# Kernel tuning notes

Hardware: AMD Instinct MI355X
Metric: run time of the kernel (lower is better)

The kernel has to match this reference:

```python
import jax, jax.numpy as jnp
import numpy as np

HID = 64
ENC_T = 20
DEC_T = 30


def lstm_cell(x, h, c, W_ih, W_hh, b_ih, b_hh):
    # PyTorch LSTMCell gate order: i, f, g, o
    gates = x @ W_ih.T + h @ W_hh.T + b_ih + b_hh  # [B, 4*HID]
    i, f, g, o = jnp.split(gates, 4, axis=-1)
    c_new = jax.nn.sigmoid(f) * c + jax.nn.sigmoid(i) * jnp.tanh(g)
    h_new = jax.nn.sigmoid(o) * jnp.tanh(c_new)
    return h_new, c_new


def setup_inputs() -> dict:
    key = jax.random.key(0)
    ks = jax.random.split(key, 11)
    B = 65536
    s_enc = 1.0 / np.sqrt(HID)
    u = lambda k, shape: jax.random.uniform(k, shape, jnp.float32, -s_enc, s_enc)
    return {
        "train_traj": jax.random.normal(ks[0], (B, ENC_T, 2), jnp.float32),
        "W_ih_enc": u(ks[1], (4 * HID, 2)),
        "W_hh_enc": u(ks[2], (4 * HID, HID)),
        "b_ih_enc": u(ks[3], (4 * HID,)),
        "b_hh_enc": u(ks[4], (4 * HID,)),
        "W_ih_dec": u(ks[5], (4 * HID, HID)),
        "W_hh_dec": u(ks[6], (4 * HID, HID)),
        "b_ih_dec": u(ks[7], (4 * HID,)),
        "b_hh_dec": u(ks[8], (4 * HID,)),
        "W_pos": u(ks[9], (2, HID)),
        "b_pos": u(ks[10], (2,)),
    }


def reference(train_traj, W_ih_enc, W_hh_enc, b_ih_enc, b_hh_enc,
              W_ih_dec, W_hh_dec, b_ih_dec, b_hh_dec, W_pos, b_pos):
    B = train_traj.shape[0]
    h0 = jnp.zeros((B, HID), train_traj.dtype)
    c0 = jnp.zeros((B, HID), train_traj.dtype)

    # Encoder: scan over the 20 time steps
    def enc_step(carry, x_t):
        h, c = carry
        h, c = lstm_cell(x_t, h, c, W_ih_enc, W_hh_enc, b_ih_enc, b_hh_enc)
        return (h, c), None

    xs = jnp.transpose(train_traj, (1, 0, 2))  # [T, B, 2]
    (h, c), _ = jax.lax.scan(enc_step, (h0, c0), xs)

    # Decoder: feed h back in as the input for 30 steps
    def dec_step(carry, _):
        h, c = carry
        h_new, c_new = lstm_cell(h, h, c, W_ih_dec, W_hh_dec, b_ih_dec, b_hh_dec)
        out = h_new @ W_pos.T + b_pos  # [B, 2]
        return (h_new, c_new), out

    (_, _), outs = jax.lax.scan(dec_step, (h, c), None, length=DEC_T)
    return jnp.transpose(outs, (1, 0, 2))  # [B, 30, 2]
```

## Files before the change

### kernel.cpp

```cpp
#include <hip/hip_runtime.h>

#define HID   64
#define ENC_T 20
#define DEC_T 30
#define ROWS  32
#define HS    72

typedef _Float16 f16;
typedef _Float16 f16x8 __attribute__((ext_vector_type(8)));
typedef _Float16 f16x4 __attribute__((ext_vector_type(4)));
typedef float  f32x4  __attribute__((ext_vector_type(4)));
typedef float  f32x2  __attribute__((ext_vector_type(2)));
typedef unsigned int   uint_t;

#if __has_builtin(__builtin_amdgcn_exp2f)
#define EXP2F(x) __builtin_amdgcn_exp2f(x)
#else
#define EXP2F(x) exp2f(x)
#endif
#if __has_builtin(__builtin_amdgcn_rcpf)
#define RCPF(x) __builtin_amdgcn_rcpf(x)
#else
#define RCPF(x) (1.0f / (x))
#endif

#define L2E 1.4426950408889634f

__device__ __forceinline__ f32x2 exp2_2(f32x2 x) {
    f32x2 r; r[0] = EXP2F(x[0]); r[1] = EXP2F(x[1]); return r;
}
__device__ __forceinline__ void batch_inv4_pk(f32x2 D0, f32x2 D1, f32x2 D2, f32x2 D3,
                                              f32x2& i0, f32x2& i1, f32x2& i2, f32x2& i3) {
    f32x2 m01 = D0 * D1;
    f32x2 m23 = D2 * D3;
    f32x2 p   = m01 * m23;
    f32x2 r;
    r[0] = RCPF(p[0]);
    r[1] = RCPF(p[1]);
    f32x2 r01 = r * m23;
    f32x2 r23 = r * m01;
    i0 = r01 * D1;
    i1 = r01 * D0;
    i2 = r23 * D3;
    i3 = r23 * D2;
}
__device__ __forceinline__ f32x4 batch_inv4(float D0, float D1, float D2, float D3) {
    float m01 = D0 * D1;
    float m23 = D2 * D3;
    float r   = RCPF(m01 * m23);
    float r01 = r * m23;
    float r23 = r * m01;
    f32x4 o;
    o[0] = r01 * D1;
    o[1] = r01 * D0;
    o[2] = r23 * D3;
    o[3] = r23 * D2;
    return o;
}

__device__ __forceinline__ f16x8 load8h(const float* __restrict__ p, float s) {
    f16x8 r;
    #pragma unroll
    for (int u = 0; u < 8; ++u) r[u] = (f16)(p[u] * s);
    return r;
}

__global__ __launch_bounds__(256, 2)
void lstm_seq2seq(const float* __restrict__ traj,
                  const float* __restrict__ WihE, const float* __restrict__ WhhE,
                  const float* __restrict__ bihE, const float* __restrict__ bhhE,
                  const float* __restrict__ WihD, const float* __restrict__ WhhD,
                  const float* __restrict__ bihD, const float* __restrict__ bhhD,
                  const float* __restrict__ Wpos, const float* __restrict__ bpos,
                  float* __restrict__ out)
{
    __shared__ __align__(16) f16   sH[2][ROWS * HS];
    __shared__ __align__(16) f16x4 sXh[ROWS * ENC_T + ENC_T];

    const int tid  = threadIdx.x;
    const int w    = tid >> 6;
    const int lane = tid & 63;
    const int col  = lane & 15;
    const int quad = lane >> 4;
    const int wg   = blockIdx.x;

    const float gsc[4] = { L2E, L2E, 2.0f * L2E, L2E };

    {
        const float* src = traj + (size_t)wg * (ROWS * ENC_T * 2);
        for (int p = tid; p < ROWS * ENC_T; p += 256) {
            f32x2 xp = *(const f32x2*)(src + 2 * p);
            f16 xh0 = (f16)xp[0], xh1 = (f16)xp[1];
            f16x4 v;
            v[0] = xh0; v[1] = xh1;
            v[2] = (f16)(xp[0] - (float)xh0);
            v[3] = (f16)(xp[1] - (float)xh1);
            sXh[p] = v;
        }
        if (tid < ENC_T) {
            f16x4 zz = {};
            sXh[ROWS * ENC_T + tid] = zz;
        }
    }
    {
        uint_t* hz = (uint_t*)&sH[0][0];
        for (int j = tid; j < ROWS * HS / 2; j += 256) hz[j] = 0;
    }

    f16x8 bw[4][3];
    #pragma unroll
    for (int j = 0; j < 4; ++j) {
        int g = 64 * j + 16 * w + col;
        #pragma unroll
        for (int kb = 0; kb < 2; ++kb)
            bw[j][kb] = load8h(WhhE + g * 64 + kb * 32 + quad * 8, gsc[j]);
        float w0 = WihE[g * 2 + 0] * gsc[j];
        float w1 = WihE[g * 2 + 1] * gsc[j];
        float bs = (bihE[g] + bhhE[g]) * gsc[j];
        f16 w0h = (f16)w0, w1h = (f16)w1, bh = (f16)bs;
        f16 w0l = (f16)(w0 - (float)w0h);
        f16 w1l = (f16)(w1 - (float)w1h);
        f16 bl  = (f16)(bs - (float)bh);
        f16x8 a2 = {};
        if (quad == 0) {
            a2[0] = w0h; a2[1] = w1h; a2[2] = w0l; a2[3] = w1l; a2[4] = bh; a2[5] = bl;
        }
        bw[j][2] = a2;
    }

    const uint_t onesd = (quad == 0) ? 0x3C003C00u : 0u;
    const int xbase0 = (quad == 0) ? (col      * ENC_T) : (ROWS * ENC_T);
    const int xbase1 = (quad == 0) ? ((col+16) * ENC_T) : (ROWS * ENC_T);
    const f32x4 z4 = { 0.f, 0.f, 0.f, 0.f };

    const f32x2 one2  = { 1.f, 1.f };
    const f32x2 two2  = { 2.f, 2.f };
    const f32x2 mone2 = { -1.f, -1.f };
    const f32x2 msc2  = { -2.f * L2E, -2.f * L2E };

    f32x2 c2[2][2] = {{{0.f,0.f},{0.f,0.f}},{{0.f,0.f},{0.f,0.f}}};
    int buf = 0;

    __syncthreads();

    for (int t = 0; t < ENC_T; ++t) {
        #pragma unroll
        for (int g = 0; g < 2; ++g) {
            const int colg = col + 16 * g;
            union { f16x4 v; uint_t d[2]; } xfu;
            xfu.v = sXh[(g ? xbase1 : xbase0) + t];
            union { f16x8 v; uint_t d[4]; } b2u;
            b2u.d[0] = xfu.d[0];
            b2u.d[1] = xfu.d[1];
            b2u.d[2] = onesd;
            b2u.d[3] = 0;
            f16x8 b0 = *(const f16x8*)&sH[buf][colg * HS +  0 + quad * 8];
            f16x8 b1 = *(const f16x8*)&sH[buf][colg * HS + 32 + quad * 8];
            f32x4 acc[4];
            #pragma unroll
            for (int j = 0; j < 4; ++j) {
                acc[j] = __builtin_amdgcn_mfma_f32_16x16x32_f16(bw[j][2], b2u.v, z4, 0, 0, 0);
                acc[j] = __builtin_amdgcn_mfma_f32_16x16x32_f16(bw[j][0], b0, acc[j], 0, 0, 0);
                acc[j] = __builtin_amdgcn_mfma_f32_16x16x32_f16(bw[j][1], b1, acc[j], 0, 0, 0);
            }
            f32x2 so2[2], cn2[2];
            #pragma unroll
            for (int rp = 0; rp < 2; ++rp) {
                f32x2 a0 = { acc[0][2*rp], acc[0][2*rp+1] };
                f32x2 a1 = { acc[1][2*rp], acc[1][2*rp+1] };
                f32x2 a2v = { acc[2][2*rp], acc[2][2*rp+1] };
                f32x2 a3 = { acc[3][2*rp], acc[3][2*rp+1] };
                f32x2 i0, i1, i2, i3;
                batch_inv4_pk(exp2_2(-a0) + one2, exp2_2(-a1) + one2,
                              exp2_2(-a2v) + one2, exp2_2(-a3) + one2,
                              i0, i1, i2, i3);
                f32x2 tg = __builtin_elementwise_fma(two2, i2, mone2);
                f32x2 cn = __builtin_elementwise_fma(i1, c2[g][rp], i0 * tg);
                c2[g][rp] = cn;
                cn2[rp] = cn;
                so2[rp] = i3;
            }
            float Dc[4];
            #pragma unroll
            for (int rp = 0; rp < 2; ++rp) {
                f32x2 xs = cn2[rp] * msc2;
                Dc[2*rp+0] = 1.f + EXP2F(fminf(fmaxf(xs[0], -30.f), 30.f));
                Dc[2*rp+1] = 1.f + EXP2F(fminf(fmaxf(xs[1], -30.f), 30.f));
            }
            f32x4 invc = batch_inv4(Dc[0], Dc[1], Dc[2], Dc[3]);
            f16x4 hh;
            #pragma unroll
            for (int rp = 0; rp < 2; ++rp) {
                f32x2 ic = { invc[2*rp], invc[2*rp+1] };
                f32x2 th = __builtin_elementwise_fma(two2, ic, mone2);
                f32x2 hn = so2[rp] * th;
                hh[2*rp+0] = (f16)hn[0];
                hh[2*rp+1] = (f16)hn[1];
            }
            *(f16x4*)&sH[buf ^ 1][colg * HS + 16 * w + quad * 4] = hh;
        }
        __syncthreads();
        buf ^= 1;
    }

    f32x4 bD4[4];
    #pragma unroll
    for (int j = 0; j < 4; ++j) {
        int g = 64 * j + 16 * w + col;
        #pragma unroll
        for (int kb = 0; kb < 2; ++kb) {
            int off = g * 64 + kb * 32 + quad * 8;
            float tmp[8];
            #pragma unroll
            for (int u = 0; u < 8; ++u) tmp[u] = WihD[off + u] + WhhD[off + u];
            bw[j][kb] = load8h(tmp, gsc[j]);
        }
        #pragma unroll
        for (int r = 0; r < 4; ++r) {
            int gr = 64 * j + 16 * w + quad * 4 + r;
            bD4[j][r] = (bihD[gr] + bhhD[gr]) * gsc[j];
        }
    }

    f16x8 wpH[2], wpL[2];
    #pragma unroll
    for (int kb = 0; kb < 2; ++kb) {
        f16x8 hv = {}, lv = {};
        if (col < 2) {
            #pragma unroll
            for (int u = 0; u < 8; ++u) {
                float v = Wpos[col * 64 + kb * 32 + quad * 8 + u];
                f16 vh = (f16)v;
                hv[u] = vh;
                lv[u] = (f16)(v - (float)vh);
            }
        }
        wpH[kb] = hv; wpL[kb] = lv;
    }
    f32x4 pinit = { 0.f, 0.f, 0.f, 0.f };
    if (quad == 0) { pinit[0] = bpos[0]; pinit[1] = bpos[1]; }

    for (int t = 0; t < DEC_T; ++t) {
        #pragma unroll
        for (int g = 0; g < 2; ++g) {
            const int colg = col + 16 * g;
            f16x8 b0 = *(const f16x8*)&sH[buf][colg * HS +  0 + quad * 8];
            f16x8 b1 = *(const f16x8*)&sH[buf][colg * HS + 32 + quad * 8];
            if (w == 0 && t > 0) {
                f32x4 pc = pinit;
                pc = __builtin_amdgcn_mfma_f32_16x16x32_f16(wpH[0], b0, pc, 0, 0, 0);
                pc = __builtin_amdgcn_mfma_f32_16x16x32_f16(wpH[1], b1, pc, 0, 0, 0);
                pc = __builtin_amdgcn_mfma_f32_16x16x32_f16(wpL[0], b0, pc, 0, 0, 0);
                pc = __builtin_amdgcn_mfma_f32_16x16x32_f16(wpL[1], b1, pc, 0, 0, 0);
                if (lane < 16) {
                    f32x2 ov = { pc[0], pc[1] };
                    *(f32x2*)&out[((size_t)(wg * ROWS + g * 16 + col)) * (DEC_T * 2) + (t - 1) * 2] = ov;
                }
            }
            f32x4 acc[4];
            #pragma unroll
            for (int j = 0; j < 4; ++j) {
                acc[j] = __builtin_amdgcn_mfma_f32_16x16x32_f16(bw[j][0], b0, bD4[j], 0, 0, 0);
                acc[j] = __builtin_amdgcn_mfma_f32_16x16x32_f16(bw[j][1], b1, acc[j], 0, 0, 0);
            }
            f32x2 so2[2], cn2[2];
            #pragma unroll
            for (int rp = 0; rp < 2; ++rp) {
                f32x2 a0 = { acc[0][2*rp], acc[0][2*rp+1] };
                f32x2 a1 = { acc[1][2*rp], acc[1][2*rp+1] };
                f32x2 a2v = { acc[2][2*rp], acc[2][2*rp+1] };
                f32x2 a3 = { acc[3][2*rp], acc[3][2*rp+1] };
                f32x2 i0, i1, i2, i3;
                batch_inv4_pk(exp2_2(-a0) + one2, exp2_2(-a1) + one2,
                              exp2_2(-a2v) + one2, exp2_2(-a3) + one2,
                              i0, i1, i2, i3);
                f32x2 tg = __builtin_elementwise_fma(two2, i2, mone2);
                f32x2 cn = __builtin_elementwise_fma(i1, c2[g][rp], i0 * tg);
                c2[g][rp] = cn;
                cn2[rp] = cn;
                so2[rp] = i3;
            }
            float Dc[4];
            #pragma unroll
            for (int rp = 0; rp < 2; ++rp) {
                f32x2 xs = cn2[rp] * msc2;
                Dc[2*rp+0] = 1.f + EXP2F(fminf(fmaxf(xs[0], -30.f), 30.f));
                Dc[2*rp+1] = 1.f + EXP2F(fminf(fmaxf(xs[1], -30.f), 30.f));
            }
            f32x4 invc = batch_inv4(Dc[0], Dc[1], Dc[2], Dc[3]);
            f16x4 hh;
            #pragma unroll
            for (int rp = 0; rp < 2; ++rp) {
                f32x2 ic = { invc[2*rp], invc[2*rp+1] };
                f32x2 th = __builtin_elementwise_fma(two2, ic, mone2);
                f32x2 hn = so2[rp] * th;
                hh[2*rp+0] = (f16)hn[0];
                hh[2*rp+1] = (f16)hn[1];
            }
            *(f16x4*)&sH[buf ^ 1][colg * HS + 16 * w + quad * 4] = hh;
        }
        __syncthreads();
        buf ^= 1;
    }

    if (w == 0) {
        #pragma unroll
        for (int g = 0; g < 2; ++g) {
            const int colg = col + 16 * g;
            f16x8 b0 = *(const f16x8*)&sH[buf][colg * HS +  0 + quad * 8];
            f16x8 b1 = *(const f16x8*)&sH[buf][colg * HS + 32 + quad * 8];
            f32x4 pc = pinit;
            pc = __builtin_amdgcn_mfma_f32_16x16x32_f16(wpH[0], b0, pc, 0, 0, 0);
            pc = __builtin_amdgcn_mfma_f32_16x16x32_f16(wpH[1], b1, pc, 0, 0, 0);
            pc = __builtin_amdgcn_mfma_f32_16x16x32_f16(wpL[0], b0, pc, 0, 0, 0);
            pc = __builtin_amdgcn_mfma_f32_16x16x32_f16(wpL[1], b1, pc, 0, 0, 0);
            if (lane < 16) {
                f32x2 ov = { pc[0], pc[1] };
                *(f32x2*)&out[((size_t)(wg * ROWS + g * 16 + col)) * (DEC_T * 2) + (DEC_T - 1) * 2] = ov;
            }
        }
    }
}

extern "C" void kernel_launch(void* const* d_in, const int* in_sizes, int n_in,
                              void* d_out, int out_size, void* d_ws, size_t ws_size,
                              hipStream_t stream) {
    const float* traj = (const float*)d_in[0];
    const float* WihE = (const float*)d_in[1];
    const float* WhhE = (const float*)d_in[2];
    const float* bihE = (const float*)d_in[3];
    const float* bhhE = (const float*)d_in[4];
    const float* WihD = (const float*)d_in[5];
    const float* WhhD = (const float*)d_in[6];
    const float* bihD = (const float*)d_in[7];
    const float* bhhD = (const float*)d_in[8];
    const float* Wpos = (const float*)d_in[9];
    const float* bpos = (const float*)d_in[10];
    float* out = (float*)d_out;

    const int B = in_sizes[0] / (ENC_T * 2);
    const int grid = B / ROWS;

    lstm_seq2seq<<<grid, 256, 0, stream>>>(traj, WihE, WhhE, bihE, bhhE,
                                           WihD, WhhD, bihD, bhhD, Wpos, bpos, out);
}
```

Baseline: 333.9 us.

## Fuse output projection into gate epilogue with fp32 FMAs and cross-wave reduction

Replaces the wave-0-only MFMA output projection (hi/lo split f16, four MFMAs per group, plus a tail pass) with per-thread fp32 FMAs on the freshly computed h values. Partial sums are reduced across quads with shuffles and across waves through a small double-buffered shared array. Sixteen lanes per wave then write the final outputs after the barrier. This removes the load imbalance where wave 0 did extra MFMA work every step, and drops the post-loop projection. In exchange every wave now does extra shuffles and shared stores each step.

Result: faster. 322.3 us (-3.5%).

```diff
diff --git a/kernel.cpp b/kernel.cpp
--- a/kernel.cpp
+++ b/kernel.cpp
@@ -76,6 +76,7 @@
 {
     __shared__ __align__(16) f16   sH[2][ROWS * HS];
     __shared__ __align__(16) f16x4 sXh[ROWS * ENC_T + ENC_T];
+    __shared__ __align__(16) float sP[2][ROWS * 8];
 
     const int tid  = threadIdx.x;
     const int w    = tid >> 6;
@@ -222,23 +223,16 @@
         }
     }
 
-    f16x8 wpH[2], wpL[2];
+    f32x2 wpA2[2], wpB2[2];
     #pragma unroll
-    for (int kb = 0; kb < 2; ++kb) {
-        f16x8 hv = {}, lv = {};
-        if (col < 2) {
-            #pragma unroll
-            for (int u = 0; u < 8; ++u) {
-                float v = Wpos[col * 64 + kb * 32 + quad * 8 + u];
-                f16 vh = (f16)v;
-                hv[u] = vh;
-                lv[u] = (f16)(v - (float)vh);
-            }
-        }
-        wpH[kb] = hv; wpL[kb] = lv;
-    }
-    f32x4 pinit = { 0.f, 0.f, 0.f, 0.f };
-    if (quad == 0) { pinit[0] = bpos[0]; pinit[1] = bpos[1]; }
+    for (int rp = 0; rp < 2; ++rp) {
+        int u = 16 * w + quad * 4 + 2 * rp;
+        wpA2[rp][0] = Wpos[u];       wpA2[rp][1] = Wpos[u + 1];
+        wpB2[rp][0] = Wpos[64 + u];  wpB2[rp][1] = Wpos[64 + u + 1];
+    }
+    const int   rrow  = w * 8 + (lane >> 1);
+    const int   rcomp = lane & 1;
+    const float bp    = bpos[rcomp];
 
     for (int t = 0; t < DEC_T; ++t) {
         #pragma unroll
@@ -246,17 +240,6 @@
             const int colg = col + 16 * g;
             f16x8 b0 = *(const f16x8*)&sH[buf][colg * HS +  0 + quad * 8];
             f16x8 b1 = *(const f16x8*)&sH[buf][colg * HS + 32 + quad * 8];
-            if (w == 0 && t > 0) {
-                f32x4 pc = pinit;
-                pc = __builtin_amdgcn_mfma_f32_16x16x32_f16(wpH[0], b0, pc, 0, 0, 0);
-                pc = __builtin_amdgcn_mfma_f32_16x16x32_f16(wpH[1], b1, pc, 0, 0, 0);
-                pc = __builtin_amdgcn_mfma_f32_16x16x32_f16(wpL[0], b0, pc, 0, 0, 0);
-                pc = __builtin_amdgcn_mfma_f32_16x16x32_f16(wpL[1], b1, pc, 0, 0, 0);
-                if (lane < 16) {
-                    f32x2 ov = { pc[0], pc[1] };
-                    *(f32x2*)&out[((size_t)(wg * ROWS + g * 16 + col)) * (DEC_T * 2) + (t - 1) * 2] = ov;
-                }
-            }
             f32x4 acc[4];
             #pragma unroll
             for (int j = 0; j < 4; ++j) {
@@ -289,35 +272,35 @@
             }
             f32x4 invc = batch_inv4(Dc[0], Dc[1], Dc[2], Dc[3]);
             f16x4 hh;
+            f32x2 pA = { 0.f, 0.f }, pB = { 0.f, 0.f };
             #pragma unroll
             for (int rp = 0; rp < 2; ++rp) {
                 f32x2 ic = { invc[2*rp], invc[2*rp+1] };
                 f32x2 th = __builtin_elementwise_fma(two2, ic, mone2);
                 f32x2 hn = so2[rp] * th;
+                pA = __builtin_elementwise_fma(hn, wpA2[rp], pA);
+                pB = __builtin_elementwise_fma(hn, wpB2[rp], pB);
                 hh[2*rp+0] = (f16)hn[0];
                 hh[2*rp+1] = (f16)hn[1];
             }
             *(f16x4*)&sH[buf ^ 1][colg * HS + 16 * w + quad * 4] = hh;
+            float p0 = pA[0] + pA[1];
+            float p1 = pB[0] + pB[1];
+            p0 += __shfl_xor(p0, 16, 64);
+            p0 += __shfl_xor(p0, 32, 64);
+            p1 += __shfl_xor(p1, 16, 64);
+            p1 += __shfl_xor(p1, 32, 64);
+            if (quad == 0) {
+                sP[buf ^ 1][colg * 8 + 0 + w] = p0;
+                sP[buf ^ 1][colg * 8 + 4 + w] = p1;
+            }
         }
         __syncthreads();
         buf ^= 1;
-    }
-
-    if (w == 0) {
-        #pragma unroll
-        for (int g = 0; g < 2; ++g) {
-            const int colg = col + 16 * g;
-            f16x8 b0 = *(const f16x8*)&sH[buf][colg * HS +  0 + quad * 8];
-            f16x8 b1 = *(const f16x8*)&sH[buf][colg * HS + 32 + quad * 8];
-            f32x4 pc = pinit;
-            pc = __builtin_amdgcn_mfma_f32_16x16x32_f16(wpH[0], b0, pc, 0, 0, 0);
-            pc = __builtin_amdgcn_mfma_f32_16x16x32_f16(wpH[1], b1, pc, 0, 0, 0);
-            pc = __builtin_amdgcn_mfma_f32_16x16x32_f16(wpL[0], b0, pc, 0, 0, 0);
-            pc = __builtin_amdgcn_mfma_f32_16x16x32_f16(wpL[1], b1, pc, 0, 0, 0);
-            if (lane < 16) {
-                f32x2 ov = { pc[0], pc[1] };
-                *(f32x2*)&out[((size_t)(wg * ROWS + g * 16 + col)) * (DEC_T * 2) + (DEC_T - 1) * 2] = ov;
-            }
+        if (lane < 16) {
+            f32x4 v = *(const f32x4*)&sP[buf][rrow * 8 + rcomp * 4];
+            float p = (v[0] + v[1]) + (v[2] + v[3]) + bp;
+            out[(size_t)(wg * ROWS + rrow) * (DEC_T * 2) + t * 2 + rcomp] = p;
         }
     }
 }
```
